# Performance work log

Hardware: AMD Instinct MI355X
Metric: run time of the kernel (lower is better)

The kernel has to match this reference:

```python
import jax, jax.numpy as jnp
import numpy as np

NUM_HEADS = 12
D_MODEL = 768
D_K = D_MODEL // NUM_HEADS


def setup_inputs() -> dict:
    key = jax.random.key(0)
    k0, k1, k2, k3, k4 = jax.random.split(key, 5)
    B, S = 4, 2048
    scale = 1.0 / np.sqrt(D_MODEL)
    return {
        "x": jax.random.normal(k0, (B, S, D_MODEL), dtype=jnp.float32),
        "wq": jax.random.normal(k1, (D_MODEL, D_MODEL), dtype=jnp.float32) * scale,
        "wk": jax.random.normal(k2, (D_MODEL, D_MODEL), dtype=jnp.float32) * scale,
        "wv": jax.random.normal(k3, (D_MODEL, D_MODEL), dtype=jnp.float32) * scale,
        "wo": jax.random.normal(k4, (D_MODEL, D_MODEL), dtype=jnp.float32) * scale,
    }


def reference(x, wq, wk, wv, wo):
    # x: [B, S, d_model]; weights are torch Linear weights [out, in], applied as x @ W^T
    B, S, _ = x.shape
    q = (x @ wq.T).reshape(B, S, NUM_HEADS, D_K).transpose(0, 2, 1, 3)  # [B,H,S,dk]
    k = (x @ wk.T).reshape(B, S, NUM_HEADS, D_K).transpose(0, 2, 1, 3)
    v = (x @ wv.T).reshape(B, S, NUM_HEADS, D_K).transpose(0, 2, 1, 3)
    # Note: original calls scaled_dot_product_attention(queries, keys, values),
    # whose body computes (first_arg @ second_arg^T) => standard Q K^T scores.
    scores = jnp.einsum("bhqd,bhkd->bhqk", q, k) / jnp.sqrt(jnp.float32(D_K))
    causal_mask = jnp.triu(jnp.ones((S, S), dtype=bool), k=1)  # True above diagonal
    scores = jnp.where(causal_mask, -jnp.inf, scores)
    probs = jax.nn.softmax(scores, axis=-1)  # stable max-subtracted softmax, as in source
    attn = jnp.einsum("bhqk,bhkd->bhqd", probs, v)  # [B,H,S,dk]
    attn = attn.transpose(0, 2, 1, 3).reshape(B, S, D_MODEL)
    return attn @ wo.T
```

## Files before the change

kernel.cpp:

```cpp
#include <hip/hip_runtime.h>
#include <stdint.h>

#define DMODEL 768
#define NHEADS 12
#define DK 64
#define BATCH 4
#define SEQ 2048
#define MTOK (BATCH*SEQ)

typedef float f32x4 __attribute__((ext_vector_type(4)));
typedef float f32x16 __attribute__((ext_vector_type(16)));
typedef short bf16x8 __attribute__((ext_vector_type(8)));
typedef unsigned short u16;
typedef unsigned int u32;

__device__ __forceinline__ u16 f2bf(float f) {
  uint32_t u = __float_as_uint(f);
  u += 0x7FFFu + ((u >> 16) & 1u);
  return (u16)(u >> 16);
}

#define GLDS16(g, l) __builtin_amdgcn_global_load_lds( \
    (const __attribute__((address_space(1))) unsigned int*)(g), \
    (__attribute__((address_space(3))) unsigned int*)(l), 16, 0, 0)

__global__ void cvt_kernel(const float* __restrict__ src, u16* __restrict__ dst, int n4) {
  int i = blockIdx.x * blockDim.x + threadIdx.x;
  if (i >= n4) return;
  float4 v = reinterpret_cast<const float4*>(src)[i];
  ushort4 o;
  o.x = f2bf(v.x); o.y = f2bf(v.y); o.z = f2bf(v.z); o.w = f2bf(v.w);
  reinterpret_cast<ushort4*>(dst)[i] = o;
}

__global__ void cvt_w4(const float* __restrict__ w0, const float* __restrict__ w1,
                       const float* __restrict__ w2, const float* __restrict__ w3,
                       u16* __restrict__ dst, int n4) {
  int i = blockIdx.x * blockDim.x + threadIdx.x;
  if (i >= n4) return;
  const float* src = (blockIdx.y == 0) ? w0 : (blockIdx.y == 1) ? w1 : (blockIdx.y == 2) ? w2 : w3;
  float4 v = reinterpret_cast<const float4*>(src)[i];
  ushort4 o;
  o.x = f2bf(v.x); o.y = f2bf(v.y); o.z = f2bf(v.z); o.w = f2bf(v.w);
  reinterpret_cast<ushort4*>(dst + (size_t)blockIdx.y * DMODEL * DMODEL)[i] = o;
}

#define BM 128
#define BN 128
#define BK 32

__device__ __forceinline__ void gemm_loop(const u16* __restrict__ A, const u16* __restrict__ W,
                                          int bm, int bn, int t, u16* As, u16* Ws,
                                          f32x4 (&acc)[2][4]) {
  const int lane = t & 63;
  const int wave = t >> 6;
  const int r16 = lane & 15, g = lane >> 4;
  const int wr = (wave >> 1) * 32;
  const int wc = (wave & 1) * 64;
  const int crow = t >> 2;
  const int cchunk = (t & 3) ^ ((t >> 3) & 3);
  const size_t aoff = (size_t)(bm + crow) * DMODEL + cchunk * 8;
  const size_t woff = (size_t)(bn + crow) * DMODEL + cchunk * 8;

  GLDS16(A + aoff, As + t * 8);
  GLDS16(W + woff, Ws + t * 8);
  __syncthreads();

  const int NK = DMODEL / BK;
  for (int kt = 0; kt < NK; ++kt) {
    const int cur = kt & 1;
    if (kt + 1 < NK) {
      GLDS16(A + aoff + (size_t)(kt + 1) * BK, As + (cur ^ 1) * 4096 + t * 8);
      GLDS16(W + woff + (size_t)(kt + 1) * BK, Ws + (cur ^ 1) * 4096 + t * 8);
    }
    bf16x8 af[2], bfr[4];
#pragma unroll
    for (int m = 0; m < 2; ++m) {
      const int row = wr + m * 16 + r16;
      af[m] = *reinterpret_cast<const bf16x8*>(&As[cur * 4096 + row * 32 + ((g ^ ((row >> 1) & 3)) * 8)]);
    }
#pragma unroll
    for (int n = 0; n < 4; ++n) {
      const int row = wc + n * 16 + r16;
      bfr[n] = *reinterpret_cast<const bf16x8*>(&Ws[cur * 4096 + row * 32 + ((g ^ ((row >> 1) & 3)) * 8)]);
    }
#pragma unroll
    for (int m = 0; m < 2; ++m)
#pragma unroll
      for (int n = 0; n < 4; ++n)
        acc[m][n] = __builtin_amdgcn_mfma_f32_16x16x32_bf16(af[m], bfr[n], acc[m][n], 0, 0, 0);
    __syncthreads();
  }
}

__launch_bounds__(512)
__global__ void qkv_gemm(const u16* __restrict__ A, const u16* __restrict__ wAll,
                         u16* __restrict__ Qw, u16* __restrict__ Kw, u16* __restrict__ Vtw) {
  __shared__ __align__(16) u16 As[2 * BM * BK];
  __shared__ __align__(16) u16 Ws[2 * BN * BK];
  const int t = threadIdx.x;
  const int lane = t & 63, wave = t >> 6;
  const int r16 = lane & 15, g = lane >> 4;
  const int bm = blockIdx.x * BM, bn = blockIdx.y * BN;
  const int z = blockIdx.z;
  const u16* W = wAll + (size_t)z * DMODEL * DMODEL;
  const int wr = (wave >> 1) * 32, wc = (wave & 1) * 64;

  f32x4 acc[2][4] = {};
  gemm_loop(A, W, bm, bn, t, As, Ws, acc);

  if (z <= 1) {
    u16* Qo = (z == 0) ? Qw : Kw;
    const float scl = (z == 0) ? 0.125f : 1.0f;
#pragma unroll
    for (int m = 0; m < 2; ++m) {
      const int gi0 = bm + wr + m * 16 + g * 4;
#pragma unroll
      for (int n = 0; n < 4; ++n) {
        const int gj = bn + wc + n * 16 + r16;
        const int h = gj >> 6, dc = gj & 63;
#pragma unroll
        for (int r = 0; r < 4; ++r) {
          const int gi = gi0 + r;
          const int b_ = gi >> 11, s = gi & 2047;
          Qo[((size_t)((b_ * NHEADS + h) * SEQ + s) << 6) + dc] = f2bf(acc[m][n][r] * scl);
        }
      }
    }
  } else {
#pragma unroll
    for (int m = 0; m < 2; ++m) {
      const int gi0 = bm + wr + m * 16 + g * 4;
      const int b_ = gi0 >> 11, s0 = gi0 & 2047;
#pragma unroll
      for (int n = 0; n < 4; ++n) {
        const int gj = bn + wc + n * 16 + r16;
        const int h = gj >> 6, dc = gj & 63;
        ushort4 pk;
        pk.x = f2bf(acc[m][n][0]); pk.y = f2bf(acc[m][n][1]);
        pk.z = f2bf(acc[m][n][2]); pk.w = f2bf(acc[m][n][3]);
        *reinterpret_cast<ushort4*>(Vtw + ((size_t)((b_ * NHEADS + h) * DK + dc) * SEQ + s0)) = pk;
      }
    }
  }
}

__launch_bounds__(512)
__global__ void out_gemm(const u16* __restrict__ A, const u16* __restrict__ W,
                         float* __restrict__ C) {
  __shared__ __align__(16) u16 As[2 * BM * BK];
  __shared__ __align__(16) u16 Ws[2 * BN * BK];
  const int t = threadIdx.x;
  const int lane = t & 63, wave = t >> 6;
  const int r16 = lane & 15, g = lane >> 4;
  const int bm = blockIdx.x * BM, bn = blockIdx.y * BN;
  const int wr = (wave >> 1) * 32, wc = (wave & 1) * 64;

  f32x4 acc[2][4] = {};
  gemm_loop(A, W, bm, bn, t, As, Ws, acc);

#pragma unroll
  for (int m = 0; m < 2; ++m) {
    const int gi0 = bm + wr + m * 16 + g * 4;
#pragma unroll
    for (int n = 0; n < 4; ++n) {
      const int gj = bn + wc + n * 16 + r16;
#pragma unroll
      for (int r = 0; r < 4; ++r)
        C[(size_t)(gi0 + r) * DMODEL + gj] = acc[m][n][r];
    }
  }
}

__device__ __forceinline__ bf16x8 mk_pa(int hi, float p0, float p1, float p2, float p3,
                                        float p4, float p5, float p6, float p7) {
  u32 w01, w23, w45, w67;
  asm("v_cvt_pk_bf16_f32 %0, %1, %2" : "=v"(w01) : "v"(p0), "v"(p1));
  asm("v_cvt_pk_bf16_f32 %0, %1, %2" : "=v"(w23) : "v"(p2), "v"(p3));
  asm("v_cvt_pk_bf16_f32 %0, %1, %2" : "=v"(w45) : "v"(p4), "v"(p5));
  asm("v_cvt_pk_bf16_f32 %0, %1, %2" : "=v"(w67) : "v"(p6), "v"(p7));
  const u32 pw01 = (u32)__shfl_xor((int)w01, 32);
  const u32 pw23 = (u32)__shfl_xor((int)w23, 32);
  const u32 pw45 = (u32)__shfl_xor((int)w45, 32);
  const u32 pw67 = (u32)__shfl_xor((int)w67, 32);
  union { u32 w[4]; bf16x8 v; } u;
  u.w[0] = hi ? pw45 : w01;
  u.w[1] = hi ? pw67 : w23;
  u.w[2] = hi ? w45  : pw01;
  u.w[3] = hi ? w67  : pw23;
  return u.v;
}

__launch_bounds__(256, 2)
__global__ void attn_kernel(const u16* __restrict__ Qg, const u16* __restrict__ Kg,
                            const u16* __restrict__ Vtg, u16* __restrict__ Og) {
  __shared__ __align__(16) u16 Ks[2][64 * 64];
  __shared__ __align__(16) u16 Vs[2][64 * 64];
  const int t = threadIdx.x;
  const int lane = t & 63, warp = t >> 6;
  const int l31 = lane & 31, hi = lane >> 5;
  const int bx = blockIdx.x;
  const int qt = 15 - (bx / 48);
  const int hb = bx % 48;
  const int h = hb % NHEADS, b = hb / NHEADS;
  const int q0w = qt * 128 + warp * 32;
  const int nt = 2 * qt + 2;
  const size_t bh = (size_t)(b * NHEADS + h);
  const u16* Qb = Qg + bh * SEQ * DK;
  const u16* Kb = Kg + bh * SEQ * DK;
  const u16* Vb = Vtg + bh * DK * SEQ;

  int srow[2], scol[2];
#pragma unroll
  for (int j = 0; j < 2; ++j) {
    const int bb = (t + j * 256) * 16;
    srow[j] = bb >> 7;
    scol[j] = ((bb & 127) ^ ((srow[j] & 7) << 4)) >> 1;
  }

  const int q = q0w + l31;
  bf16x8 qf[4];
#pragma unroll
  for (int kk = 0; kk < 4; ++kk)
    qf[kk] = *reinterpret_cast<const bf16x8*>(Qb + (size_t)q * DK + kk * 16 + hi * 8);

  f32x16 o0 = {}, o1 = {};
  float m = -__builtin_inff(), l = 0.f;
  const int hi4 = hi * 4;
  const int xr = (l31 & 7) << 4;

#pragma unroll
  for (int j = 0; j < 2; ++j) {
    GLDS16(Kb + (size_t)srow[j] * DK + scol[j], &Ks[0][0] + (t + j * 256) * 8);
    GLDS16(Vb + (size_t)srow[j] * SEQ + scol[j], &Vs[0][0] + (t + j * 256) * 8);
  }
  __syncthreads();

  for (int i = 0; i < nt; ++i) {
    const int cur = i & 1;
    const int kv0 = i * 64;
    if (i + 1 < nt) {
      const int nkv0 = kv0 + 64;
#pragma unroll
      for (int j = 0; j < 2; ++j) {
        GLDS16(Kb + (size_t)(nkv0 + srow[j]) * DK + scol[j], &Ks[cur ^ 1][0] + (t + j * 256) * 8);
        GLDS16(Vb + (size_t)srow[j] * SEQ + nkv0 + scol[j], &Vs[cur ^ 1][0] + (t + j * 256) * 8);
      }
    }

    if (kv0 <= q0w + 31) {
      f32x16 t0 = {}, t1 = {};
      const char* Kc = (const char*)Ks[cur];
#pragma unroll
      for (int kk = 0; kk < 4; ++kk) {
        const int cb = kk * 32 + hi * 16;
        bf16x8 a0 = *reinterpret_cast<const bf16x8*>(Kc + ((l31 * 128 + cb) ^ xr));
        bf16x8 a1 = *reinterpret_cast<const bf16x8*>(Kc + (((l31 + 32) * 128 + cb) ^ xr));
        t0 = __builtin_amdgcn_mfma_f32_32x32x16_bf16(a0, qf[kk], t0, 0, 0, 0);
        t1 = __builtin_amdgcn_mfma_f32_32x32x16_bf16(a1, qf[kk], t1, 0, 0, 0);
      }

      if (kv0 + 63 > q0w) {
        const int qmh = (q - kv0) - hi4;
#pragma unroll
        for (int r = 0; r < 16; ++r) {
          const int kvc = (r & 3) + 8 * (r >> 2);
          if (kvc > qmh)      t0[r] = -__builtin_inff();
          if (kvc + 32 > qmh) t1[r] = -__builtin_inff();
        }
      }

      float x0 = fmaxf(t0[0], t0[1]),  x1 = fmaxf(t0[2], t0[3]);
      float x2 = fmaxf(t0[4], t0[5]),  x3 = fmaxf(t0[6], t0[7]);
      float x4 = fmaxf(t0[8], t0[9]),  x5 = fmaxf(t0[10], t0[11]);
      float x6 = fmaxf(t0[12], t0[13]), x7 = fmaxf(t0[14], t0[15]);
      x0 = fmaxf(x0, x1); x2 = fmaxf(x2, x3); x4 = fmaxf(x4, x5); x6 = fmaxf(x6, x7);
      float y0 = fmaxf(t1[0], t1[1]),  y1 = fmaxf(t1[2], t1[3]);
      float y2 = fmaxf(t1[4], t1[5]),  y3 = fmaxf(t1[6], t1[7]);
      float y4 = fmaxf(t1[8], t1[9]),  y5 = fmaxf(t1[10], t1[11]);
      float y6 = fmaxf(t1[12], t1[13]), y7 = fmaxf(t1[14], t1[15]);
      y0 = fmaxf(y0, y1); y2 = fmaxf(y2, y3); y4 = fmaxf(y4, y5); y6 = fmaxf(y6, y7);
      float pm = fmaxf(fmaxf(fmaxf(x0, x2), fmaxf(x4, x6)),
                       fmaxf(fmaxf(y0, y2), fmaxf(y4, y6)));
      pm = fmaxf(pm, __shfl_xor(pm, 32));

      if (pm > m) {
        const float corr = __expf(m - pm);
        l *= corr;
        o0 = o0 * corr;
        o1 = o1 * corr;
        m = pm;
      }

#pragma unroll
      for (int r = 0; r < 16; ++r) { t0[r] = __expf(t0[r] - m); }
#pragma unroll
      for (int r = 0; r < 16; ++r) { t1[r] = __expf(t1[r] - m); }
      float s0 = 0.f, s1 = 0.f, s2 = 0.f, s3 = 0.f;
#pragma unroll
      for (int r = 0; r < 4; ++r) {
        s0 += t0[r]; s1 += t0[4 + r]; s2 += t0[8 + r]; s3 += t0[12 + r];
        s0 += t1[r]; s1 += t1[4 + r]; s2 += t1[8 + r]; s3 += t1[12 + r];
      }
      float s = (s0 + s1) + (s2 + s3);
      l += s + __shfl_xor(s, 32);

      bf16x8 pa0 = mk_pa(hi, t0[0], t0[1], t0[2], t0[3], t0[4], t0[5], t0[6], t0[7]);
      bf16x8 pa1 = mk_pa(hi, t0[8], t0[9], t0[10], t0[11], t0[12], t0[13], t0[14], t0[15]);
      bf16x8 pa2 = mk_pa(hi, t1[0], t1[1], t1[2], t1[3], t1[4], t1[5], t1[6], t1[7]);
      bf16x8 pa3 = mk_pa(hi, t1[8], t1[9], t1[10], t1[11], t1[12], t1[13], t1[14], t1[15]);

      const char* Vc = (const char*)Vs[cur];
#pragma unroll
      for (int ks = 0; ks < 4; ++ks) {
        const int cb = ks * 32 + hi * 16;
        bf16x8 v0 = *reinterpret_cast<const bf16x8*>(Vc + ((l31 * 128 + cb) ^ xr));
        bf16x8 v1 = *reinterpret_cast<const bf16x8*>(Vc + (((l31 + 32) * 128 + cb) ^ xr));
        const bf16x8 pk = (ks == 0) ? pa0 : (ks == 1) ? pa1 : (ks == 2) ? pa2 : pa3;
        o0 = __builtin_amdgcn_mfma_f32_32x32x16_bf16(v0, pk, o0, 0, 0, 0);
        o1 = __builtin_amdgcn_mfma_f32_32x32x16_bf16(v1, pk, o1, 0, 0, 0);
      }
    }
    __syncthreads();
  }

  const float rinv = 1.0f / l;
  u16* orow = Og + (size_t)(b * SEQ + q) * DMODEL + h * 64;
#pragma unroll
  for (int j = 0; j < 4; ++j) {
    ushort4 pk;
    pk.x = f2bf(o0[4 * j + 0] * rinv); pk.y = f2bf(o0[4 * j + 1] * rinv);
    pk.z = f2bf(o0[4 * j + 2] * rinv); pk.w = f2bf(o0[4 * j + 3] * rinv);
    *reinterpret_cast<ushort4*>(orow + 8 * j + hi4) = pk;
  }
#pragma unroll
  for (int j = 0; j < 4; ++j) {
    ushort4 pk;
    pk.x = f2bf(o1[4 * j + 0] * rinv); pk.y = f2bf(o1[4 * j + 1] * rinv);
    pk.z = f2bf(o1[4 * j + 2] * rinv); pk.w = f2bf(o1[4 * j + 3] * rinv);
    *reinterpret_cast<ushort4*>(orow + 32 + 8 * j + hi4) = pk;
  }
}

extern "C" void kernel_launch(void* const* d_in, const int* in_sizes, int n_in,
                              void* d_out, int out_size, void* d_ws, size_t ws_size,
                              hipStream_t stream) {
  const float* x  = (const float*)d_in[0];
  const float* wq = (const float*)d_in[1];
  const float* wk = (const float*)d_in[2];
  const float* wv = (const float*)d_in[3];
  const float* wo = (const float*)d_in[4];

  const size_t SZ_TOK = (size_t)MTOK * DMODEL * 2;
  const size_t SZ_W   = (size_t)DMODEL * DMODEL * 2;
  char* ws = (char*)d_ws;
  size_t off = 0;
  u16* xb  = (u16*)(ws + off); off += SZ_TOK;
  u16* wqb = (u16*)(ws + off); off += 4 * SZ_W;
  u16* Qw  = (u16*)(ws + off); off += SZ_TOK;
  u16* Kw  = (u16*)(ws + off); off += SZ_TOK;
  u16* Vtw = (u16*)(ws + off); off += SZ_TOK;
  u16* Ow  = (u16*)(ws + off); off += SZ_TOK;
  if (ws_size < off) return;
  u16* wob = wqb + 3 * (size_t)DMODEL * DMODEL;

  const int nx4 = MTOK * DMODEL / 4;
  const int nw4 = DMODEL * DMODEL / 4;
  cvt_kernel<<<nx4 / 256, 256, 0, stream>>>(x, xb, nx4);
  cvt_w4<<<dim3(nw4 / 256, 4), 256, 0, stream>>>(wq, wk, wv, wo, wqb, nw4);

  qkv_gemm<<<dim3(MTOK / BM, DMODEL / BN, 3), 512, 0, stream>>>(xb, wqb, Qw, Kw, Vtw);

  attn_kernel<<<dim3(768), 256, 0, stream>>>(Qw, Kw, Vtw, Ow);

  out_gemm<<<dim3(MTOK / BM, DMODEL / BN), 512, 0, stream>>>(Ow, wob, (float*)d_out);
}
```

Before: 205.6 us.

## Use 4-wave GEMM blocks with larger per-wave tiles, exp2 softmax, MFMA priority

The GEMMs now run 256-thread blocks where each wave computes a 64x64 tile, with each thread issuing two async loads per operand. This gives more data reuse per wave but fewer waves per block. The Q projection scale now folds in log2(e), so the attention softmax can use the native exp2 instead of __expf. The attention MFMA sections are also wrapped in s_setprio raises so the matrix work gets issue priority over other waves.

```diff
diff --git a/kernel.cpp b/kernel.cpp
--- a/kernel.cpp
+++ b/kernel.cpp
@@ -13,6 +13,8 @@
 typedef short bf16x8 __attribute__((ext_vector_type(8)));
 typedef unsigned short u16;
 typedef unsigned int u32;
+
+#define LOG2E 1.4426950408889634f
 
 __device__ __forceinline__ u16 f2bf(float f) {
   uint32_t u = __float_as_uint(f);
@@ -51,31 +53,37 @@
 
 __device__ __forceinline__ void gemm_loop(const u16* __restrict__ A, const u16* __restrict__ W,
                                           int bm, int bn, int t, u16* As, u16* Ws,
-                                          f32x4 (&acc)[2][4]) {
+                                          f32x4 (&acc)[4][4]) {
   const int lane = t & 63;
   const int wave = t >> 6;
   const int r16 = lane & 15, g = lane >> 4;
-  const int wr = (wave >> 1) * 32;
+  const int wr = (wave >> 1) * 64;
   const int wc = (wave & 1) * 64;
-  const int crow = t >> 2;
-  const int cchunk = (t & 3) ^ ((t >> 3) & 3);
-  const size_t aoff = (size_t)(bm + crow) * DMODEL + cchunk * 8;
-  const size_t woff = (size_t)(bn + crow) * DMODEL + cchunk * 8;
-
-  GLDS16(A + aoff, As + t * 8);
-  GLDS16(W + woff, Ws + t * 8);
+  const int c0 = t, c1 = t + 256;
+  const int r0 = c0 >> 2, k0 = ((c0 & 3) ^ ((c0 >> 3) & 3)) * 8;
+  const int r1 = c1 >> 2, k1 = ((c1 & 3) ^ ((c1 >> 3) & 3)) * 8;
+  const size_t a0 = (size_t)(bm + r0) * DMODEL + k0;
+  const size_t a1 = (size_t)(bm + r1) * DMODEL + k1;
+  const size_t w0 = (size_t)(bn + r0) * DMODEL + k0;
+  const size_t w1 = (size_t)(bn + r1) * DMODEL + k1;
+
+  GLDS16(A + a0, As + c0 * 8); GLDS16(A + a1, As + c1 * 8);
+  GLDS16(W + w0, Ws + c0 * 8); GLDS16(W + w1, Ws + c1 * 8);
   __syncthreads();
 
   const int NK = DMODEL / BK;
   for (int kt = 0; kt < NK; ++kt) {
     const int cur = kt & 1;
     if (kt + 1 < NK) {
-      GLDS16(A + aoff + (size_t)(kt + 1) * BK, As + (cur ^ 1) * 4096 + t * 8);
-      GLDS16(W + woff + (size_t)(kt + 1) * BK, Ws + (cur ^ 1) * 4096 + t * 8);
-    }
-    bf16x8 af[2], bfr[4];
-#pragma unroll
-    for (int m = 0; m < 2; ++m) {
+      const size_t koff = (size_t)(kt + 1) * BK;
+      GLDS16(A + a0 + koff, As + (cur ^ 1) * 4096 + c0 * 8);
+      GLDS16(A + a1 + koff, As + (cur ^ 1) * 4096 + c1 * 8);
+      GLDS16(W + w0 + koff, Ws + (cur ^ 1) * 4096 + c0 * 8);
+      GLDS16(W + w1 + koff, Ws + (cur ^ 1) * 4096 + c1 * 8);
+    }
+    bf16x8 af[4], bfr[4];
+#pragma unroll
+    for (int m = 0; m < 4; ++m) {
       const int row = wr + m * 16 + r16;
       af[m] = *reinterpret_cast<const bf16x8*>(&As[cur * 4096 + row * 32 + ((g ^ ((row >> 1) & 3)) * 8)]);
     }
@@ -85,7 +93,7 @@
       bfr[n] = *reinterpret_cast<const bf16x8*>(&Ws[cur * 4096 + row * 32 + ((g ^ ((row >> 1) & 3)) * 8)]);
     }
 #pragma unroll
-    for (int m = 0; m < 2; ++m)
+    for (int m = 0; m < 4; ++m)
 #pragma unroll
       for (int n = 0; n < 4; ++n)
         acc[m][n] = __builtin_amdgcn_mfma_f32_16x16x32_bf16(af[m], bfr[n], acc[m][n], 0, 0, 0);
@@ -93,7 +101,7 @@
   }
 }
 
-__launch_bounds__(512)
+__launch_bounds__(256)
 __global__ void qkv_gemm(const u16* __restrict__ A, const u16* __restrict__ wAll,
                          u16* __restrict__ Qw, u16* __restrict__ Kw, u16* __restrict__ Vtw) {
   __shared__ __align__(16) u16 As[2 * BM * BK];
@@ -104,16 +112,16 @@
   const int bm = blockIdx.x * BM, bn = blockIdx.y * BN;
   const int z = blockIdx.z;
   const u16* W = wAll + (size_t)z * DMODEL * DMODEL;
-  const int wr = (wave >> 1) * 32, wc = (wave & 1) * 64;
-
-  f32x4 acc[2][4] = {};
+  const int wr = (wave >> 1) * 64, wc = (wave & 1) * 64;
+
+  f32x4 acc[4][4] = {};
   gemm_loop(A, W, bm, bn, t, As, Ws, acc);
 
   if (z <= 1) {
     u16* Qo = (z == 0) ? Qw : Kw;
-    const float scl = (z == 0) ? 0.125f : 1.0f;
-#pragma unroll
-    for (int m = 0; m < 2; ++m) {
+    const float scl = (z == 0) ? (0.125f * LOG2E) : 1.0f;
+#pragma unroll
+    for (int m = 0; m < 4; ++m) {
       const int gi0 = bm + wr + m * 16 + g * 4;
 #pragma unroll
       for (int n = 0; n < 4; ++n) {
@@ -129,7 +137,7 @@
     }
   } else {
 #pragma unroll
-    for (int m = 0; m < 2; ++m) {
+    for (int m = 0; m < 4; ++m) {
       const int gi0 = bm + wr + m * 16 + g * 4;
       const int b_ = gi0 >> 11, s0 = gi0 & 2047;
 #pragma unroll
@@ -145,7 +153,7 @@
   }
 }
 
-__launch_bounds__(512)
+__launch_bounds__(256)
 __global__ void out_gemm(const u16* __restrict__ A, const u16* __restrict__ W,
                          float* __restrict__ C) {
   __shared__ __align__(16) u16 As[2 * BM * BK];
@@ -154,13 +162,13 @@
   const int lane = t & 63, wave = t >> 6;
   const int r16 = lane & 15, g = lane >> 4;
   const int bm = blockIdx.x * BM, bn = blockIdx.y * BN;
-  const int wr = (wave >> 1) * 32, wc = (wave & 1) * 64;
-
-  f32x4 acc[2][4] = {};
+  const int wr = (wave >> 1) * 64, wc = (wave & 1) * 64;
+
+  f32x4 acc[4][4] = {};
   gemm_loop(A, W, bm, bn, t, As, Ws, acc);
 
 #pragma unroll
-  for (int m = 0; m < 2; ++m) {
+  for (int m = 0; m < 4; ++m) {
     const int gi0 = bm + wr + m * 16 + g * 4;
 #pragma unroll
     for (int n = 0; n < 4; ++n) {
@@ -251,6 +259,7 @@
     if (kv0 <= q0w + 31) {
       f32x16 t0 = {}, t1 = {};
       const char* Kc = (const char*)Ks[cur];
+      __builtin_amdgcn_s_setprio(1);
 #pragma unroll
       for (int kk = 0; kk < 4; ++kk) {
         const int cb = kk * 32 + hi * 16;
@@ -259,6 +268,7 @@
         t0 = __builtin_amdgcn_mfma_f32_32x32x16_bf16(a0, qf[kk], t0, 0, 0, 0);
         t1 = __builtin_amdgcn_mfma_f32_32x32x16_bf16(a1, qf[kk], t1, 0, 0, 0);
       }
+      __builtin_amdgcn_s_setprio(0);
 
       if (kv0 + 63 > q0w) {
         const int qmh = (q - kv0) - hi4;
@@ -285,7 +295,7 @@
       pm = fmaxf(pm, __shfl_xor(pm, 32));
 
       if (pm > m) {
-        const float corr = __expf(m - pm);
+        const float corr = __builtin_amdgcn_exp2f(m - pm);
         l *= corr;
         o0 = o0 * corr;
         o1 = o1 * corr;
@@ -293,9 +303,9 @@
       }
 
 #pragma unroll
-      for (int r = 0; r < 16; ++r) { t0[r] = __expf(t0[r] - m); }
-#pragma unroll
-      for (int r = 0; r < 16; ++r) { t1[r] = __expf(t1[r] - m); }
+      for (int r = 0; r < 16; ++r) { t0[r] = __builtin_amdgcn_exp2f(t0[r] - m); }
+#pragma unroll
+      for (int r = 0; r < 16; ++r) { t1[r] = __builtin_amdgcn_exp2f(t1[r] - m); }
       float s0 = 0.f, s1 = 0.f, s2 = 0.f, s3 = 0.f;
 #pragma unroll
       for (int r = 0; r < 4; ++r) {
@@ -311,6 +321,7 @@
       bf16x8 pa3 = mk_pa(hi, t1[8], t1[9], t1[10], t1[11], t1[12], t1[13], t1[14], t1[15]);
 
       const char* Vc = (const char*)Vs[cur];
+      __builtin_amdgcn_s_setprio(1);
 #pragma unroll
       for (int ks = 0; ks < 4; ++ks) {
         const int cb = ks * 32 + hi * 16;
@@ -320,6 +331,7 @@
         o0 = __builtin_amdgcn_mfma_f32_32x32x16_bf16(v0, pk, o0, 0, 0, 0);
         o1 = __builtin_amdgcn_mfma_f32_32x32x16_bf16(v1, pk, o1, 0, 0, 0);
       }
+      __builtin_amdgcn_s_setprio(0);
     }
     __syncthreads();
   }
@@ -369,9 +381,9 @@
   cvt_kernel<<<nx4 / 256, 256, 0, stream>>>(x, xb, nx4);
   cvt_w4<<<dim3(nw4 / 256, 4), 256, 0, stream>>>(wq, wk, wv, wo, wqb, nw4);
 
-  qkv_gemm<<<dim3(MTOK / BM, DMODEL / BN, 3), 512, 0, stream>>>(xb, wqb, Qw, Kw, Vtw);
+  qkv_gemm<<<dim3(MTOK / BM, DMODEL / BN, 3), 256, 0, stream>>>(xb, wqb, Qw, Kw, Vtw);
 
   attn_kernel<<<dim3(768), 256, 0, stream>>>(Qw, Kw, Vtw, Ow);
 
-  out_gemm<<<dim3(MTOK / BM, DMODEL / BN), 512, 0, stream>>>(Ow, wob, (float*)d_out);
-}
+  out_gemm<<<dim3(MTOK / BM, DMODEL / BN), 256, 0, stream>>>(Ow, wob, (float*)d_out);
+}
```

After: 211.3 us. 1.03x slower.

## Merge conversion kernels, use exp2 softmax with lazy rescale and MFMA priority

Applied to the files above, without the earlier changes.

Merges the x and weight bf16 conversion kernels into one launch. Folds log2(e) into the Q scaling so the softmax can use the hardware exp2 instruction directly. Rescales the running max only when some lane's max grows by more than 8 (in log2 units), which skips most correction multiplies on the accumulators. Also rewrites the max reduction with three-input max chains and raises wave priority around the MFMA blocks. The lazy rescale lets probabilities exceed 1 by up to 2^8 before bf16 packing, a small numerical-range risk.

```diff
diff --git a/kernel.cpp b/kernel.cpp
--- a/kernel.cpp
+++ b/kernel.cpp
@@ -14,6 +14,8 @@
 typedef unsigned short u16;
 typedef unsigned int u32;
 
+#define LOG2E 1.4426950408889634f
+
 __device__ __forceinline__ u16 f2bf(float f) {
   uint32_t u = __float_as_uint(f);
   u += 0x7FFFu + ((u >> 16) & 1u);
@@ -24,25 +26,27 @@
     (const __attribute__((address_space(1))) unsigned int*)(g), \
     (__attribute__((address_space(3))) unsigned int*)(l), 16, 0, 0)
 
-__global__ void cvt_kernel(const float* __restrict__ src, u16* __restrict__ dst, int n4) {
+__global__ void cvt_all(const float* __restrict__ x,
+                        const float* __restrict__ wq, const float* __restrict__ wk,
+                        const float* __restrict__ wv, const float* __restrict__ wo,
+                        u16* __restrict__ xb, u16* __restrict__ wb) {
+  const int NX = MTOK * DMODEL / 4;
+  const int NW = DMODEL * DMODEL / 4;
   int i = blockIdx.x * blockDim.x + threadIdx.x;
-  if (i >= n4) return;
-  float4 v = reinterpret_cast<const float4*>(src)[i];
+  const float* src; u16* dst; int idx;
+  if (i < NX) {
+    src = x; dst = xb; idx = i;
+  } else {
+    const int j = i - NX;
+    const int w = j / NW;
+    idx = j - w * NW;
+    src = (w == 0) ? wq : (w == 1) ? wk : (w == 2) ? wv : wo;
+    dst = wb + (size_t)w * DMODEL * DMODEL;
+  }
+  float4 v = reinterpret_cast<const float4*>(src)[idx];
   ushort4 o;
   o.x = f2bf(v.x); o.y = f2bf(v.y); o.z = f2bf(v.z); o.w = f2bf(v.w);
-  reinterpret_cast<ushort4*>(dst)[i] = o;
-}
-
-__global__ void cvt_w4(const float* __restrict__ w0, const float* __restrict__ w1,
-                       const float* __restrict__ w2, const float* __restrict__ w3,
-                       u16* __restrict__ dst, int n4) {
-  int i = blockIdx.x * blockDim.x + threadIdx.x;
-  if (i >= n4) return;
-  const float* src = (blockIdx.y == 0) ? w0 : (blockIdx.y == 1) ? w1 : (blockIdx.y == 2) ? w2 : w3;
-  float4 v = reinterpret_cast<const float4*>(src)[i];
-  ushort4 o;
-  o.x = f2bf(v.x); o.y = f2bf(v.y); o.z = f2bf(v.z); o.w = f2bf(v.w);
-  reinterpret_cast<ushort4*>(dst + (size_t)blockIdx.y * DMODEL * DMODEL)[i] = o;
+  reinterpret_cast<ushort4*>(dst)[idx] = o;
 }
 
 #define BM 128
@@ -111,7 +115,7 @@
 
   if (z <= 1) {
     u16* Qo = (z == 0) ? Qw : Kw;
-    const float scl = (z == 0) ? 0.125f : 1.0f;
+    const float scl = (z == 0) ? (0.125f * LOG2E) : 1.0f;
 #pragma unroll
     for (int m = 0; m < 2; ++m) {
       const int gi0 = bm + wr + m * 16 + g * 4;
@@ -189,6 +193,10 @@
   u.w[2] = hi ? w45  : pw01;
   u.w[3] = hi ? w67  : pw23;
   return u.v;
+}
+
+__device__ __forceinline__ float max3f(float a, float b, float c) {
+  return fmaxf(fmaxf(a, b), c);
 }
 
 __launch_bounds__(256, 2)
@@ -251,6 +259,7 @@
     if (kv0 <= q0w + 31) {
       f32x16 t0 = {}, t1 = {};
       const char* Kc = (const char*)Ks[cur];
+      __builtin_amdgcn_s_setprio(1);
 #pragma unroll
       for (int kk = 0; kk < 4; ++kk) {
         const int cb = kk * 32 + hi * 16;
@@ -259,6 +268,7 @@
         t0 = __builtin_amdgcn_mfma_f32_32x32x16_bf16(a0, qf[kk], t0, 0, 0, 0);
         t1 = __builtin_amdgcn_mfma_f32_32x32x16_bf16(a1, qf[kk], t1, 0, 0, 0);
       }
+      __builtin_amdgcn_s_setprio(0);
 
       if (kv0 + 63 > q0w) {
         const int qmh = (q - kv0) - hi4;
@@ -270,32 +280,37 @@
         }
       }
 
-      float x0 = fmaxf(t0[0], t0[1]),  x1 = fmaxf(t0[2], t0[3]);
-      float x2 = fmaxf(t0[4], t0[5]),  x3 = fmaxf(t0[6], t0[7]);
-      float x4 = fmaxf(t0[8], t0[9]),  x5 = fmaxf(t0[10], t0[11]);
-      float x6 = fmaxf(t0[12], t0[13]), x7 = fmaxf(t0[14], t0[15]);
-      x0 = fmaxf(x0, x1); x2 = fmaxf(x2, x3); x4 = fmaxf(x4, x5); x6 = fmaxf(x6, x7);
-      float y0 = fmaxf(t1[0], t1[1]),  y1 = fmaxf(t1[2], t1[3]);
-      float y2 = fmaxf(t1[4], t1[5]),  y3 = fmaxf(t1[6], t1[7]);
-      float y4 = fmaxf(t1[8], t1[9]),  y5 = fmaxf(t1[10], t1[11]);
-      float y6 = fmaxf(t1[12], t1[13]), y7 = fmaxf(t1[14], t1[15]);
-      y0 = fmaxf(y0, y1); y2 = fmaxf(y2, y3); y4 = fmaxf(y4, y5); y6 = fmaxf(y6, y7);
-      float pm = fmaxf(fmaxf(fmaxf(x0, x2), fmaxf(x4, x6)),
-                       fmaxf(fmaxf(y0, y2), fmaxf(y4, y6)));
+      float a0_ = max3f(t0[0], t0[1], t0[2]);
+      float a1_ = max3f(t0[3], t0[4], t0[5]);
+      float a2_ = max3f(t0[6], t0[7], t0[8]);
+      float a3_ = max3f(t0[9], t0[10], t0[11]);
+      float a4_ = max3f(t0[12], t0[13], t0[14]);
+      float a5_ = max3f(t0[15], t1[0], t1[1]);
+      float a6_ = max3f(t1[2], t1[3], t1[4]);
+      float a7_ = max3f(t1[5], t1[6], t1[7]);
+      float a8_ = max3f(t1[8], t1[9], t1[10]);
+      float a9_ = max3f(t1[11], t1[12], t1[13]);
+      float aa_ = fmaxf(t1[14], t1[15]);
+      float b0_ = max3f(a0_, a1_, a2_);
+      float b1_ = max3f(a3_, a4_, a5_);
+      float b2_ = max3f(a6_, a7_, a8_);
+      float b3_ = max3f(a9_, aa_, b0_);
+      float pm = max3f(b1_, b2_, b3_);
       pm = fmaxf(pm, __shfl_xor(pm, 32));
 
-      if (pm > m) {
-        const float corr = __expf(m - pm);
+      if (__any(pm > m + 8.f)) {
+        const float mnew = fmaxf(m, pm);
+        const float corr = __builtin_amdgcn_exp2f(m - mnew);
         l *= corr;
         o0 = o0 * corr;
         o1 = o1 * corr;
-        m = pm;
-      }
-
-#pragma unroll
-      for (int r = 0; r < 16; ++r) { t0[r] = __expf(t0[r] - m); }
-#pragma unroll
-      for (int r = 0; r < 16; ++r) { t1[r] = __expf(t1[r] - m); }
+        m = mnew;
+      }
+
+#pragma unroll
+      for (int r = 0; r < 16; ++r) { t0[r] = __builtin_amdgcn_exp2f(t0[r] - m); }
+#pragma unroll
+      for (int r = 0; r < 16; ++r) { t1[r] = __builtin_amdgcn_exp2f(t1[r] - m); }
       float s0 = 0.f, s1 = 0.f, s2 = 0.f, s3 = 0.f;
 #pragma unroll
       for (int r = 0; r < 4; ++r) {
@@ -311,6 +326,7 @@
       bf16x8 pa3 = mk_pa(hi, t1[8], t1[9], t1[10], t1[11], t1[12], t1[13], t1[14], t1[15]);
 
       const char* Vc = (const char*)Vs[cur];
+      __builtin_amdgcn_s_setprio(1);
 #pragma unroll
       for (int ks = 0; ks < 4; ++ks) {
         const int cb = ks * 32 + hi * 16;
@@ -320,6 +336,7 @@
         o0 = __builtin_amdgcn_mfma_f32_32x32x16_bf16(v0, pk, o0, 0, 0, 0);
         o1 = __builtin_amdgcn_mfma_f32_32x32x16_bf16(v1, pk, o1, 0, 0, 0);
       }
+      __builtin_amdgcn_s_setprio(0);
     }
     __syncthreads();
   }
@@ -364,10 +381,9 @@
   if (ws_size < off) return;
   u16* wob = wqb + 3 * (size_t)DMODEL * DMODEL;
 
-  const int nx4 = MTOK * DMODEL / 4;
-  const int nw4 = DMODEL * DMODEL / 4;
-  cvt_kernel<<<nx4 / 256, 256, 0, stream>>>(x, xb, nx4);
-  cvt_w4<<<dim3(nw4 / 256, 4), 256, 0, stream>>>(wq, wk, wv, wo, wqb, nw4);
+  const int NX = MTOK * DMODEL / 4;
+  const int NW = DMODEL * DMODEL / 4;
+  cvt_all<<<(NX + 4 * NW) / 256, 256, 0, stream>>>(x, wq, wk, wv, wo, xb, wqb);
 
   qkv_gemm<<<dim3(MTOK / BM, DMODEL / BN, 3), 512, 0, stream>>>(xb, wqb, Qw, Kw, Vtw);
 
```

After: 198.7 us. 1.03x faster.
